# Optimization experiments

Measured on AMD Instinct MI355X. Metric: run time of the kernel, lower is better.

## Reference

```python
import jax, jax.numpy as jnp
import numpy as np
import math

BLUR, P, SCALING = 0.05, 2.0, 0.9
DIAMETER = 8.0  # static bound on max |x-y| for unit-normal 1-D data (geomloss derives it from data)
NEG = -1e9     # masked log-weight


def _eps_schedule():
    # geomloss epsilon_schedule: diameter^p -> blur^p, geometric with ratio scaling^p
    eps = [DIAMETER ** P]
    eps += list(np.exp(np.arange(P * math.log(DIAMETER), P * math.log(BLUR), P * math.log(SCALING))))
    eps += [BLUR ** P]
    return np.asarray(eps, dtype=np.float32)


def _softmin(eps, C, h):
    # h: [m] = log-weights + dual/eps ; returns [n] = -eps*logsumexp_j(h_j - C_ij/eps)
    return -eps * jax.nn.logsumexp(h[None, :] - C / eps, axis=1)


def _sinkhorn_divergence(x, y, logw):
    # x, y: [B] 1-D point clouds for one output dim; logw: [B] masked log-weights.
    # Debiased Sinkhorn divergence S = OT_eps(a,b) - 0.5 OT(a,a) - 0.5 OT(b,b), p=2 cost |x-y|^2/2.
    Cxy = 0.5 * (x[:, None] - y[None, :]) ** 2
    Cxx = 0.5 * (x[:, None] - x[None, :]) ** 2
    Cyy = 0.5 * (y[:, None] - y[None, :]) ** 2
    eps_list = jnp.asarray(_eps_schedule())
    e0 = eps_list[0]
    f = _softmin(e0, Cxy, logw)    # dual on x for OT(a,b)
    g = _softmin(e0, Cxy.T, logw)  # dual on y for OT(a,b)
    a = _softmin(e0, Cxx, logw)    # self dual on x
    b = _softmin(e0, Cyy, logw)    # self dual on y

    def step(carry, eps):
        f, g, a, b = carry
        ft = _softmin(eps, Cxy, logw + g / eps)
        gt = _softmin(eps, Cxy.T, logw + f / eps)
        at = _softmin(eps, Cxx, logw + a / eps)
        bt = _softmin(eps, Cyy, logw + b / eps)
        return (0.5 * (f + ft), 0.5 * (g + gt), 0.5 * (a + at), 0.5 * (b + bt)), None

    (f, g, a, b), _ = jax.lax.scan(step, (f, g, a, b), eps_list)
    # last extrapolation at final eps (full updates, no damping)
    e = eps_list[-1]
    f, g = _softmin(e, Cxy, logw + g / e), _softmin(e, Cxy.T, logw + f / e)
    a = 0.5 * (a + _softmin(e, Cxx, logw + a / e))
    b = 0.5 * (b + _softmin(e, Cyy, logw + b / e))
    w = jnp.exp(logw)  # 1/n on valid samples, 0 on masked
    return jnp.sum(w * (f - a)) + jnp.sum(w * (g - b))


def reference(predictions, targets):
    # predictions, targets: [B, D]; NaNs in targets mark invalid samples per dim
    mask = ~jnp.isnan(targets)                      # [B, D]
    y = jnp.where(mask, targets, 0.0)
    counts = jnp.sum(mask, axis=0)                  # [D]
    logn = jnp.log(jnp.maximum(counts, 1).astype(predictions.dtype))
    logw = jnp.where(mask, -logn[None, :], NEG)     # [B, D]
    per_dim = jax.vmap(_sinkhorn_divergence, in_axes=(1, 1, 1))(predictions, y, logw)
    per_dim = jnp.where(counts > 1, per_dim, 0.0)   # dims with <=1 valid sample -> 0
    total = jnp.mean(per_dim)                       # weights=None -> mean over dims
    return total, per_dim


def setup_inputs() -> dict:
    key = jax.random.key(0)
    k1, k2, k3 = jax.random.split(key, 3)
    B, D = 2048, 8
    preds = jax.random.normal(k1, (B, D), dtype=jnp.float32)
    targ = jax.random.normal(k2, (B, D), dtype=jnp.float32)
    nan_mask = jax.random.uniform(k3, (B, D)) < 0.1
    targ = jnp.where(nan_mask, jnp.nan, targ)
    return {"predictions": preds, "targets": targ}
```

## Files before the change

### kernel.cpp

```cpp
#include <hip/hip_runtime.h>
#include <math.h>

#define BN 2048
#define DN 8
#define NEGW -1e9f
#define TPB 256
#define RPB 128
#define RS 32
#define JSPLIT 8
#define SLOTS (BN/2)
#define SPC (SLOTS/JSPLIT)

typedef float f2 __attribute__((ext_vector_type(2)));

static __device__ __forceinline__ float wave_reduce_sum(float v){
  #pragma unroll
  for (int off = 32; off > 0; off >>= 1) v += __shfl_xor(v, off, 64);
  return v;
}

__global__ void setup_kernel(const float* __restrict__ pred, const float* __restrict__ targ,
                             float* __restrict__ xcol, float* __restrict__ ycol,
                             float* __restrict__ logw, float* __restrict__ counts){
  int d = blockIdx.x;
  int t = threadIdx.x;
  int lane = t & 63, wave = t >> 6;
  float mk[BN/256];
  float c = 0.f;
  for (int k = 0; k < BN/256; k++){
    int i = t + k*256;
    float tv = targ[i*DN + d];
    bool m = !(tv != tv);
    mk[k] = m ? 1.f : 0.f;
    c += mk[k];
    ycol[d*BN + i] = m ? tv : 0.f;
    xcol[d*BN + i] = pred[i*DN + d];
  }
  __shared__ float sh[4];
  __shared__ float logn_sh;
  float cw = wave_reduce_sum(c);
  if (lane == 0) sh[wave] = cw;
  __syncthreads();
  if (t == 0){
    float tot = sh[0] + sh[1] + sh[2] + sh[3];
    counts[d] = tot;
    logn_sh = logf(fmaxf(tot, 1.f));
  }
  __syncthreads();
  float ln = logn_sh;
  for (int k = 0; k < BN/256; k++){
    int i = t + k*256;
    logw[d*BN + i] = (mk[k] > 0.f) ? -ln : NEGW;
  }
}

__global__ __launch_bounds__(TPB) void sink_step(
      const float* __restrict__ xcol, const float* __restrict__ ycol,
      const float* __restrict__ logw,
      const float* __restrict__ dold, float* __restrict__ dnew,
      float eps, float inv_eps, int mode){
  const float L2E = 1.44269504088896340736f;
  const float LN2 = 0.69314718055994530942f;
  __shared__ float4 pair4[SLOTS];
  __shared__ float pm[JSPLIT][RPB];
  __shared__ float ps[JSPLIT][RPB];
  __shared__ float mmx[RPB];

  int bid = blockIdx.x;
  int rc  = bid & 15;
  int mat = (bid >> 4) & 3;
  int d   = bid >> 6;
  int t   = threadIdx.x;
  int rs  = t & (RS-1);
  int jc  = t >> 5;

  const float* xb = xcol + d*BN;
  const float* yb = ycol + d*BN;
  const float* lw = logw + d*BN;
  const float* ri; const float* pj; int hsel;
  switch (mat){
    case 0:  ri = xb; pj = yb; hsel = 1; break;
    case 1:  ri = yb; pj = xb; hsel = 0; break;
    case 2:  ri = xb; pj = xb; hsel = 2; break;
    default: ri = yb; pj = yb; hsel = 3; break;
  }
  const float* hd  = dold + (size_t)hsel*DN*BN + d*BN;
  const float* dmp = dold + (size_t)mat *DN*BN + d*BN;
  float*       op  = dnew + (size_t)mat *DN*BN + d*BN;

  const float c1 = L2E * inv_eps;
  const float c2 = 0.5f * inv_eps * L2E;

  const float2* pj2 = (const float2*)pj;
  const float2* lw2 = (const float2*)lw;
  const float2* hd2 = (const float2*)hd;
  #pragma unroll
  for (int k = 0; k < SLOTS/TPB; k++){
    int idx = t + k*TPB;
    float2 y2 = pj2[idx];
    float2 l2 = lw2[idx];
    float h0 = l2.x, h1 = l2.y;
    if (mode != 0){
      float2 dd = hd2[idx];
      h0 = fmaf(dd.x, inv_eps, h0);
      h1 = fmaf(dd.y, inv_eps, h1);
    }
    pair4[idx] = make_float4(y2.x, y2.y,
                             fmaf(-c2*y2.x, y2.x, L2E*h0),
                             fmaf(-c2*y2.y, y2.y, L2E*h1));
  }

  int row0 = rc*RPB + rs;
  f2 a2[4];
  #pragma unroll
  for (int r = 0; r < 4; r++){
    float xi = ri[row0 + 32*r];
    float al = c1 * xi;
    a2[r] = (f2){al, al};
  }
  __syncthreads();

  int q0 = jc * SPC;
  f2 m2[4];
  #pragma unroll
  for (int r = 0; r < 4; r++) m2[r] = (f2){-INFINITY, -INFINITY};
  #pragma unroll 1
  for (int q = 0; q < SPC; q += 8){
    float4 P0 = pair4[q0+q+0]; float4 P1 = pair4[q0+q+1];
    float4 P2 = pair4[q0+q+2]; float4 P3 = pair4[q0+q+3];
    float4 P4 = pair4[q0+q+4]; float4 P5 = pair4[q0+q+5];
    float4 P6 = pair4[q0+q+6]; float4 P7 = pair4[q0+q+7];
    #pragma unroll
    for (int r = 0; r < 4; r++){
      f2 a = a2[r], mm = m2[r];
      mm = __builtin_elementwise_max(mm, __builtin_elementwise_fma(a, (f2){P0.x,P0.y}, (f2){P0.z,P0.w}));
      mm = __builtin_elementwise_max(mm, __builtin_elementwise_fma(a, (f2){P1.x,P1.y}, (f2){P1.z,P1.w}));
      mm = __builtin_elementwise_max(mm, __builtin_elementwise_fma(a, (f2){P2.x,P2.y}, (f2){P2.z,P2.w}));
      mm = __builtin_elementwise_max(mm, __builtin_elementwise_fma(a, (f2){P3.x,P3.y}, (f2){P3.z,P3.w}));
      mm = __builtin_elementwise_max(mm, __builtin_elementwise_fma(a, (f2){P4.x,P4.y}, (f2){P4.z,P4.w}));
      mm = __builtin_elementwise_max(mm, __builtin_elementwise_fma(a, (f2){P5.x,P5.y}, (f2){P5.z,P5.w}));
      mm = __builtin_elementwise_max(mm, __builtin_elementwise_fma(a, (f2){P6.x,P6.y}, (f2){P6.z,P6.w}));
      mm = __builtin_elementwise_max(mm, __builtin_elementwise_fma(a, (f2){P7.x,P7.y}, (f2){P7.z,P7.w}));
      m2[r] = mm;
    }
  }
  #pragma unroll
  for (int r = 0; r < 4; r++) pm[jc][rs + 32*r] = fmaxf(m2[r].x, m2[r].y);
  __syncthreads();

  if (t < RPB){
    float m = -INFINITY;
    #pragma unroll
    for (int k = 0; k < JSPLIT; k++) m = fmaxf(m, pm[k][t]);
    mmx[t] = m;
  }
  __syncthreads();

  f2 mb[4];
  #pragma unroll
  for (int r = 0; r < 4; r++){
    float m = mmx[rs + 32*r];
    mb[r] = (f2){m, m};
  }

  f2 s2[4];
  #pragma unroll
  for (int r = 0; r < 4; r++) s2[r] = (f2){0.f, 0.f};
  #pragma unroll 1
  for (int q = 0; q < SPC; q += 8){
    float4 P0 = pair4[q0+q+0]; float4 P1 = pair4[q0+q+1];
    float4 P2 = pair4[q0+q+2]; float4 P3 = pair4[q0+q+3];
    float4 P4 = pair4[q0+q+4]; float4 P5 = pair4[q0+q+5];
    float4 P6 = pair4[q0+q+6]; float4 P7 = pair4[q0+q+7];
    #pragma unroll
    for (int r = 0; r < 4; r++){
      f2 a = a2[r], m = mb[r], ss = s2[r];
      f2 v;
      v = __builtin_elementwise_fma(a, (f2){P0.x,P0.y}, (f2){P0.z,P0.w}) - m;
      ss += (f2){__builtin_amdgcn_exp2f(v.x), __builtin_amdgcn_exp2f(v.y)};
      v = __builtin_elementwise_fma(a, (f2){P1.x,P1.y}, (f2){P1.z,P1.w}) - m;
      ss += (f2){__builtin_amdgcn_exp2f(v.x), __builtin_amdgcn_exp2f(v.y)};
      v = __builtin_elementwise_fma(a, (f2){P2.x,P2.y}, (f2){P2.z,P2.w}) - m;
      ss += (f2){__builtin_amdgcn_exp2f(v.x), __builtin_amdgcn_exp2f(v.y)};
      v = __builtin_elementwise_fma(a, (f2){P3.x,P3.y}, (f2){P3.z,P3.w}) - m;
      ss += (f2){__builtin_amdgcn_exp2f(v.x), __builtin_amdgcn_exp2f(v.y)};
      v = __builtin_elementwise_fma(a, (f2){P4.x,P4.y}, (f2){P4.z,P4.w}) - m;
      ss += (f2){__builtin_amdgcn_exp2f(v.x), __builtin_amdgcn_exp2f(v.y)};
      v = __builtin_elementwise_fma(a, (f2){P5.x,P5.y}, (f2){P5.z,P5.w}) - m;
      ss += (f2){__builtin_amdgcn_exp2f(v.x), __builtin_amdgcn_exp2f(v.y)};
      v = __builtin_elementwise_fma(a, (f2){P6.x,P6.y}, (f2){P6.z,P6.w}) - m;
      ss += (f2){__builtin_amdgcn_exp2f(v.x), __builtin_amdgcn_exp2f(v.y)};
      v = __builtin_elementwise_fma(a, (f2){P7.x,P7.y}, (f2){P7.z,P7.w}) - m;
      ss += (f2){__builtin_amdgcn_exp2f(v.x), __builtin_amdgcn_exp2f(v.y)};
      s2[r] = ss;
    }
  }
  #pragma unroll
  for (int r = 0; r < 4; r++) ps[jc][rs + 32*r] = s2[r].x + s2[r].y;
  __syncthreads();

  if (t < RPB){
    int row = rc*RPB + t;
    float s = 0.f;
    #pragma unroll
    for (int k = 0; k < JSPLIT; k++) s += ps[k][t];
    float m  = mmx[t];
    float xi = ri[row];
    float beta = c2 * xi * xi;
    float lse2 = (m + __builtin_amdgcn_logf(s)) - beta;
    float tn = -eps * (LN2 * lse2);
    float outv;
    if (mode == 1 || (mode == 2 && mat >= 2)) outv = 0.5f * (dmp[row] + tn);
    else                                      outv = tn;
    op[row] = outv;
  }
}

__global__ void reduce_kernel(const float* __restrict__ dual, const float* __restrict__ logw,
                              const float* __restrict__ counts, float* __restrict__ out){
  int d = blockIdx.x;
  int t = threadIdx.x;
  int lane = t & 63, wave = t >> 6;
  float acc = 0.f;
  for (int k = 0; k < BN/256; k++){
    int i = t + k*256;
    float w  = expf(logw[d*BN + i]);
    float fv = dual[0*DN*BN + d*BN + i];
    float gv = dual[1*DN*BN + d*BN + i];
    float av = dual[2*DN*BN + d*BN + i];
    float bv = dual[3*DN*BN + d*BN + i];
    acc += w * ((fv - av) + (gv - bv));
  }
  __shared__ float sh[4];
  float aw = wave_reduce_sum(acc);
  if (lane == 0) sh[wave] = aw;
  __syncthreads();
  if (t == 0){
    float tot = sh[0] + sh[1] + sh[2] + sh[3];
    out[1 + d] = (counts[d] > 1.5f) ? tot : 0.f;
  }
}

__global__ void total_kernel(float* __restrict__ out){
  if (threadIdx.x == 0 && blockIdx.x == 0){
    float s = 0.f;
    for (int d = 0; d < DN; d++) s += out[1 + d];
    out[0] = s / (float)DN;
  }
}

extern "C" void kernel_launch(void* const* d_in, const int* in_sizes, int n_in,
                              void* d_out, int out_size, void* d_ws, size_t ws_size,
                              hipStream_t stream){
  const float* pred = (const float*)d_in[0];
  const float* targ = (const float*)d_in[1];
  float* out = (float*)d_out;
  float* ws  = (float*)d_ws;

  float* xcol   = ws;
  float* ycol   = ws + (size_t)DN*BN;
  float* logw   = ws + (size_t)2*DN*BN;
  float* counts = ws + (size_t)3*DN*BN;
  float* buf0   = ws + (size_t)3*DN*BN + 64;
  float* buf1   = buf0 + (size_t)4*DN*BN;

  float eps_list[64]; int n = 0;
  {
    const double P = 2.0, DIAM = 8.0, BLUR = 0.05, SC = 0.9;
    double ls = P*log(DIAM), le = P*log(BLUR), st = P*log(SC);
    eps_list[n++] = (float)pow(DIAM, P);
    int cnt = (int)ceil((le - ls)/st);
    for (int k = 0; k < cnt; k++) eps_list[n++] = (float)exp(ls + st*(double)k);
    eps_list[n++] = (float)(BLUR*BLUR);
  }

  setup_kernel<<<DN, 256, 0, stream>>>(pred, targ, xcol, ycol, logw, counts);

  dim3 grid(DN*4*16), blk(TPB);
  float* cur = buf0; float* nxt = buf1;
  {
    float e = eps_list[0];
    sink_step<<<grid, blk, 0, stream>>>(xcol, ycol, logw, cur, cur, e, 1.f/e, 0);
  }
  for (int k = 0; k < n; k++){
    float e = eps_list[k];
    sink_step<<<grid, blk, 0, stream>>>(xcol, ycol, logw, cur, nxt, e, 1.f/e, 1);
    float* tmp = cur; cur = nxt; nxt = tmp;
  }
  {
    float e = eps_list[n-1];
    sink_step<<<grid, blk, 0, stream>>>(xcol, ycol, logw, cur, nxt, e, 1.f/e, 2);
    float* tmp = cur; cur = nxt; nxt = tmp;
  }
  reduce_kernel<<<DN, 256, 0, stream>>>(cur, logw, counts, out);
  total_kernel<<<1, 64, 0, stream>>>(out);
}
```

Baseline: 1.142 ms.

## Halve rows per block, double j-split, and pad shared pair buffer

Each block now handles 64 rows instead of 128 and splits the column range across 16 thread groups instead of 8, so the grid doubles to 1024 blocks. The aim is to fill more of the MI355X's compute units. The shared pair buffer is padded by one float4 every 64 entries so that different column chunks start on different LDS banks. In exchange, each block redoes the full staging of the 1024 pair entries into shared memory for half as many rows, which doubles the total staging work and global reads per launch.

Result: no change. 1.130 ms (-1.1%).

```diff
diff --git a/kernel.cpp b/kernel.cpp
--- a/kernel.cpp
+++ b/kernel.cpp
@@ -5,11 +5,12 @@
 #define DN 8
 #define NEGW -1e9f
 #define TPB 256
-#define RPB 128
-#define RS 32
-#define JSPLIT 8
+#define RPB 64
+#define RS 16
+#define JSPLIT 16
 #define SLOTS (BN/2)
 #define SPC (SLOTS/JSPLIT)
+#define CPAD 65
 
 typedef float f2 __attribute__((ext_vector_type(2)));
 
@@ -61,18 +62,18 @@
       float eps, float inv_eps, int mode){
   const float L2E = 1.44269504088896340736f;
   const float LN2 = 0.69314718055994530942f;
-  __shared__ float4 pair4[SLOTS];
+  __shared__ float4 pair4[JSPLIT*CPAD];
   __shared__ float pm[JSPLIT][RPB];
   __shared__ float ps[JSPLIT][RPB];
   __shared__ float mmx[RPB];
 
   int bid = blockIdx.x;
-  int rc  = bid & 15;
-  int mat = (bid >> 4) & 3;
-  int d   = bid >> 6;
+  int rc  = bid & 31;
+  int mat = (bid >> 5) & 3;
+  int d   = bid >> 7;
   int t   = threadIdx.x;
   int rs  = t & (RS-1);
-  int jc  = t >> 5;
+  int jc  = t >> 4;
 
   const float* xb = xcol + d*BN;
   const float* yb = ycol + d*BN;
@@ -97,6 +98,7 @@
   #pragma unroll
   for (int k = 0; k < SLOTS/TPB; k++){
     int idx = t + k*TPB;
+    int phys = idx + (idx >> 6);
     float2 y2 = pj2[idx];
     float2 l2 = lw2[idx];
     float h0 = l2.x, h1 = l2.y;
@@ -105,31 +107,31 @@
       h0 = fmaf(dd.x, inv_eps, h0);
       h1 = fmaf(dd.y, inv_eps, h1);
     }
-    pair4[idx] = make_float4(y2.x, y2.y,
-                             fmaf(-c2*y2.x, y2.x, L2E*h0),
-                             fmaf(-c2*y2.y, y2.y, L2E*h1));
+    pair4[phys] = make_float4(y2.x, y2.y,
+                              fmaf(-c2*y2.x, y2.x, L2E*h0),
+                              fmaf(-c2*y2.y, y2.y, L2E*h1));
   }
 
   int row0 = rc*RPB + rs;
   f2 a2[4];
   #pragma unroll
   for (int r = 0; r < 4; r++){
-    float xi = ri[row0 + 32*r];
+    float xi = ri[row0 + RS*r];
     float al = c1 * xi;
     a2[r] = (f2){al, al};
   }
   __syncthreads();
 
-  int q0 = jc * SPC;
+  const float4* cb = pair4 + jc*CPAD;
   f2 m2[4];
   #pragma unroll
   for (int r = 0; r < 4; r++) m2[r] = (f2){-INFINITY, -INFINITY};
   #pragma unroll 1
   for (int q = 0; q < SPC; q += 8){
-    float4 P0 = pair4[q0+q+0]; float4 P1 = pair4[q0+q+1];
-    float4 P2 = pair4[q0+q+2]; float4 P3 = pair4[q0+q+3];
-    float4 P4 = pair4[q0+q+4]; float4 P5 = pair4[q0+q+5];
-    float4 P6 = pair4[q0+q+6]; float4 P7 = pair4[q0+q+7];
+    float4 P0 = cb[q+0]; float4 P1 = cb[q+1];
+    float4 P2 = cb[q+2]; float4 P3 = cb[q+3];
+    float4 P4 = cb[q+4]; float4 P5 = cb[q+5];
+    float4 P6 = cb[q+6]; float4 P7 = cb[q+7];
     #pragma unroll
     for (int r = 0; r < 4; r++){
       f2 a = a2[r], mm = m2[r];
@@ -145,7 +147,7 @@
     }
   }
   #pragma unroll
-  for (int r = 0; r < 4; r++) pm[jc][rs + 32*r] = fmaxf(m2[r].x, m2[r].y);
+  for (int r = 0; r < 4; r++) pm[jc][rs + RS*r] = fmaxf(m2[r].x, m2[r].y);
   __syncthreads();
 
   if (t < RPB){
@@ -159,7 +161,7 @@
   f2 mb[4];
   #pragma unroll
   for (int r = 0; r < 4; r++){
-    float m = mmx[rs + 32*r];
+    float m = mmx[rs + RS*r];
     mb[r] = (f2){m, m};
   }
 
@@ -168,10 +170,10 @@
   for (int r = 0; r < 4; r++) s2[r] = (f2){0.f, 0.f};
   #pragma unroll 1
   for (int q = 0; q < SPC; q += 8){
-    float4 P0 = pair4[q0+q+0]; float4 P1 = pair4[q0+q+1];
-    float4 P2 = pair4[q0+q+2]; float4 P3 = pair4[q0+q+3];
-    float4 P4 = pair4[q0+q+4]; float4 P5 = pair4[q0+q+5];
-    float4 P6 = pair4[q0+q+6]; float4 P7 = pair4[q0+q+7];
+    float4 P0 = cb[q+0]; float4 P1 = cb[q+1];
+    float4 P2 = cb[q+2]; float4 P3 = cb[q+3];
+    float4 P4 = cb[q+4]; float4 P5 = cb[q+5];
+    float4 P6 = cb[q+6]; float4 P7 = cb[q+7];
     #pragma unroll
     for (int r = 0; r < 4; r++){
       f2 a = a2[r], m = mb[r], ss = s2[r];
@@ -196,7 +198,7 @@
     }
   }
   #pragma unroll
-  for (int r = 0; r < 4; r++) ps[jc][rs + 32*r] = s2[r].x + s2[r].y;
+  for (int r = 0; r < 4; r++) ps[jc][rs + RS*r] = s2[r].x + s2[r].y;
   __syncthreads();
 
   if (t < RPB){
@@ -276,7 +278,7 @@
 
   setup_kernel<<<DN, 256, 0, stream>>>(pred, targ, xcol, ycol, logw, counts);
 
-  dim3 grid(DN*4*16), blk(TPB);
+  dim3 grid(DN*4*32), blk(TPB);
   float* cur = buf0; float* nxt = buf1;
   {
     float e = eps_list[0];
```
